# Optimization experiments

Hardware: AMD Instinct MI355X
Metric: run time of the kernel (lower is better)

Reference implementation:

```python
import jax, jax.numpy as jnp
import numpy as np


def setup_inputs() -> dict:
    key = jax.random.key(0)
    k1, k2 = jax.random.split(key)
    B, S, R, F = 256, 64, 128, 1536
    tri_feat_org = jax.random.normal(k1, (B, R, F), dtype=jnp.float32)
    alpha = jax.random.uniform(k2, (B, S, R), dtype=jnp.float32)
    mask = jnp.ones((B, S), dtype=jnp.float32)
    return {"tri_feat_org": tri_feat_org, "alpha": alpha, "mask": mask}


def reference(tri_feat_org, alpha, mask):
    # tri_feat_org: (B, R, 1536); alpha: (B, S, R); mask: (B, S)
    B, R, F = tri_feat_org.shape
    D = F // 6  # 256
    numtrue = jnp.sum(mask)
    # (alpha - 0.1) * mask, broadcast over rel dim (matches torch broadcasting;
    # the original's mask.expand_as(alpha) result is discarded)
    a = (alpha - 0.1) * mask[:, :, None]  # (B, S, R)

    # Slicing layout: h=[0:512], r=[512:1024], t=[1024:1536]; each split re/im 256
    h_re = tri_feat_org[..., 0 * D:1 * D]
    h_im = tri_feat_org[..., 1 * D:2 * D]
    r_re = tri_feat_org[..., 2 * D:3 * D]
    r_im = tri_feat_org[..., 3 * D:4 * D]
    t_re = tri_feat_org[..., 4 * D:5 * D]
    t_im = tri_feat_org[..., 5 * D:6 * D]

    # ComplEx score on the UNSCALED features; since alpha is constant across the
    # feature dim, (a*h)*(a*t)*(a*r) = a^3 * (h*t*r), so we never materialize
    # the (B,S,R,1536) expanded tensor the torch code builds.
    s0 = jnp.sum(h_re * t_re * r_re + h_im * t_im * r_re
                 + h_re * t_im * r_im - h_im * t_re * r_im, axis=-1)  # (B, R)
    score = -(a ** 3) * s0[:, None, :]  # (B, S, R)

    # regul: mean over (B,S,R,D) of (a * feat_slice)^2 for each of the 6 slices.
    # Factor as sum_{b,r} (sum_s a^2) * (sum_d feat^2) / (B*S*R*D).
    a2s = jnp.sum(a ** 2, axis=1)  # (B, R)
    S_len = a.shape[1]
    denom = jnp.asarray(B * S_len * R * D, dtype=tri_feat_org.dtype)

    def slice_mean_sq(f):
        return jnp.sum(a2s * jnp.sum(f ** 2, axis=-1)) / denom

    regul = (slice_mean_sq(h_re) + slice_mean_sq(h_im)
             + slice_mean_sq(t_re) + slice_mean_sq(t_im)
             + slice_mean_sq(r_re) + slice_mean_sq(r_im))

    output = jnp.sum(jax.nn.softplus(score)) / numtrue + 0.01 * regul
    return output
```

## Files before the change

### kernel.cpp

```cpp
#include <hip/hip_runtime.h>

constexpr int Bc = 256;
constexpr int Sc = 64;
constexpr int Rc = 128;
constexpr int Fc = 1536;
constexpr int Dc = 256;

__device__ __forceinline__ void accum_term(float h_re, float h_im,
                                           float r_re, float r_im,
                                           float t_re, float t_im,
                                           float& s0, float& q) {
  s0 += r_re * (h_re * t_re + h_im * t_im) + r_im * (h_re * t_im - h_im * t_re);
  q  += h_re * h_re + h_im * h_im + r_re * r_re + r_im * r_im + t_re * t_re + t_im * t_im;
}

__global__ __launch_bounds__(256) void rowstats_kernel(
    const float* __restrict__ tri, float* __restrict__ s0_out,
    float* __restrict__ q_out) {
  const int wid  = threadIdx.x >> 6;
  const int lane = threadIdx.x & 63;
  const int row  = blockIdx.x * 4 + wid;

  const float4* p4 = reinterpret_cast<const float4*>(tri + (size_t)row * Fc);
  const float4 hre = p4[lane +   0];
  const float4 him = p4[lane +  64];
  const float4 rre = p4[lane + 128];
  const float4 rim = p4[lane + 192];
  const float4 tre = p4[lane + 256];
  const float4 tim = p4[lane + 320];

  float s0 = 0.f, q = 0.f;
  accum_term(hre.x, him.x, rre.x, rim.x, tre.x, tim.x, s0, q);
  accum_term(hre.y, him.y, rre.y, rim.y, tre.y, tim.y, s0, q);
  accum_term(hre.z, him.z, rre.z, rim.z, tre.z, tim.z, s0, q);
  accum_term(hre.w, him.w, rre.w, rim.w, tre.w, tim.w, s0, q);

  #pragma unroll
  for (int off = 32; off > 0; off >>= 1) {
    s0 += __shfl_down(s0, off, 64);
    q  += __shfl_down(q, off, 64);
  }
  if (lane == 0) {
    s0_out[row] = s0;
    q_out[row]  = q;
  }
}

__global__ __launch_bounds__(256) void score_kernel(
    const float* __restrict__ alpha, const float* __restrict__ mask,
    const float* __restrict__ s0_arr, const float* __restrict__ q_arr,
    double* __restrict__ acc) {
  const int t   = blockIdx.x * 256 + threadIdx.x;
  const int idx = t * 4;
  const int r   = idx & (Rc - 1);
  const int bs  = idx >> 7;
  const int b   = bs >> 6;

  const float m = mask[bs];
  const float4 al  = *reinterpret_cast<const float4*>(alpha + idx);
  const float4 s0v = *reinterpret_cast<const float4*>(s0_arr + b * Rc + r);
  const float4 qv  = *reinterpret_cast<const float4*>(q_arr + b * Rc + r);

  float sp_sum = 0.f, aq_sum = 0.f;
  {
    float a = (al.x - 0.1f) * m;
    float sc = -(a * a * a) * s0v.x;
    sp_sum += fmaxf(sc, 0.f) + log1pf(__expf(-fabsf(sc)));
    aq_sum += a * a * qv.x;
  }
  {
    float a = (al.y - 0.1f) * m;
    float sc = -(a * a * a) * s0v.y;
    sp_sum += fmaxf(sc, 0.f) + log1pf(__expf(-fabsf(sc)));
    aq_sum += a * a * qv.y;
  }
  {
    float a = (al.z - 0.1f) * m;
    float sc = -(a * a * a) * s0v.z;
    sp_sum += fmaxf(sc, 0.f) + log1pf(__expf(-fabsf(sc)));
    aq_sum += a * a * qv.z;
  }
  {
    float a = (al.w - 0.1f) * m;
    float sc = -(a * a * a) * s0v.w;
    sp_sum += fmaxf(sc, 0.f) + log1pf(__expf(-fabsf(sc)));
    aq_sum += a * a * qv.w;
  }

  #pragma unroll
  for (int off = 32; off > 0; off >>= 1) {
    sp_sum += __shfl_down(sp_sum, off, 64);
    aq_sum += __shfl_down(aq_sum, off, 64);
  }
  __shared__ float lds[8];
  const int lane = threadIdx.x & 63, wid = threadIdx.x >> 6;
  if (lane == 0) {
    lds[wid]     = sp_sum;
    lds[wid + 4] = aq_sum;
  }
  __syncthreads();
  if (threadIdx.x == 0) {
    float spb = lds[0] + lds[1] + lds[2] + lds[3];
    float aqb = lds[4] + lds[5] + lds[6] + lds[7];
    atomicAdd(acc + 0, (double)spb);
    atomicAdd(acc + 1, (double)aqb);
  }
}

__global__ __launch_bounds__(256) void finalize_kernel(
    const float* __restrict__ mask, const double* __restrict__ acc,
    float* __restrict__ out) {
  float s = 0.f;
  for (int i = threadIdx.x; i < Bc * Sc; i += 256) s += mask[i];
  #pragma unroll
  for (int off = 32; off > 0; off >>= 1) s += __shfl_down(s, off, 64);
  __shared__ float lds[4];
  const int lane = threadIdx.x & 63, wid = threadIdx.x >> 6;
  if (lane == 0) lds[wid] = s;
  __syncthreads();
  if (threadIdx.x == 0) {
    double numtrue = (double)(lds[0] + lds[1] + lds[2] + lds[3]);
    double denom   = (double)Bc * (double)Sc * (double)Rc * (double)Dc;
    out[0] = (float)(acc[0] / numtrue + 0.01 * acc[1] / denom);
  }
}

extern "C" void kernel_launch(void* const* d_in, const int* in_sizes, int n_in,
                              void* d_out, int out_size, void* d_ws, size_t ws_size,
                              hipStream_t stream) {
  const float* tri   = (const float*)d_in[0];
  const float* alpha = (const float*)d_in[1];
  const float* mask  = (const float*)d_in[2];
  float* out = (float*)d_out;

  double* acc    = (double*)d_ws;
  float*  s0_arr = (float*)((char*)d_ws + 64);
  float*  q_arr  = s0_arr + Bc * Rc;

  hipMemsetAsync(d_ws, 0, 64, stream);

  rowstats_kernel<<<(Bc * Rc) / 4, 256, 0, stream>>>(tri, s0_arr, q_arr);
  score_kernel<<<(Bc * Sc * Rc) / (4 * 256), 256, 0, stream>>>(alpha, mask, s0_arr,
                                                               q_arr, acc);
  finalize_kernel<<<1, 256, 0, stream>>>(mask, acc, out);
}
```

Measured before the change: 342.5 us.

## Fuse rowstats, score and finalize into one kernel with last-block reduction

Merges the three kernels into a single launch. Each block computes row statistics for 16 relations of one batch into shared memory, then applies them to the matching alpha tile. The final mask sum and output are computed by the last block to finish, detected with an atomic counter. This removes the global intermediate arrays and two launch boundaries, at the cost of fewer blocks (2048), a serialized finalize tail, and per-block atomics.

```diff
diff --git a/kernel.cpp b/kernel.cpp
--- a/kernel.cpp
+++ b/kernel.cpp
@@ -5,6 +5,7 @@
 constexpr int Rc = 128;
 constexpr int Fc = 1536;
 constexpr int Dc = 256;
+
 
 __device__ __forceinline__ void accum_term(float h_re, float h_im,
                                            float r_re, float r_im,
@@ -14,77 +15,63 @@
   q  += h_re * h_re + h_im * h_im + r_re * r_re + r_im * r_im + t_re * t_re + t_im * t_im;
 }
 
-__global__ __launch_bounds__(256) void rowstats_kernel(
-    const float* __restrict__ tri, float* __restrict__ s0_out,
-    float* __restrict__ q_out) {
+__global__ __launch_bounds__(256) void fused_kernel(
+    const float* __restrict__ tri, const float* __restrict__ alpha,
+    const float* __restrict__ mask, double* __restrict__ acc,
+    unsigned int* __restrict__ counter, float* __restrict__ out) {
   const int wid  = threadIdx.x >> 6;
   const int lane = threadIdx.x & 63;
-  const int row  = blockIdx.x * 4 + wid;
+  const int b     = blockIdx.x >> 3;
+  const int r0    = (blockIdx.x & 7) * 16;
 
-  const float4* p4 = reinterpret_cast<const float4*>(tri + (size_t)row * Fc);
-  const float4 hre = p4[lane +   0];
-  const float4 him = p4[lane +  64];
-  const float4 rre = p4[lane + 128];
-  const float4 rim = p4[lane + 192];
-  const float4 tre = p4[lane + 256];
-  const float4 tim = p4[lane + 320];
-
-  float s0 = 0.f, q = 0.f;
-  accum_term(hre.x, him.x, rre.x, rim.x, tre.x, tim.x, s0, q);
-  accum_term(hre.y, him.y, rre.y, rim.y, tre.y, tim.y, s0, q);
-  accum_term(hre.z, him.z, rre.z, rim.z, tre.z, tim.z, s0, q);
-  accum_term(hre.w, him.w, rre.w, rim.w, tre.w, tim.w, s0, q);
+  __shared__ float s0_lds[16];
+  __shared__ float q_lds[16];
 
   #pragma unroll
-  for (int off = 32; off > 0; off >>= 1) {
-    s0 += __shfl_down(s0, off, 64);
-    q  += __shfl_down(q, off, 64);
+  for (int j = 0; j < 4; ++j) {
+    const int r = r0 + wid * 4 + j;
+    const float4* p4 =
+        reinterpret_cast<const float4*>(tri + ((size_t)b * Rc + r) * Fc);
+    const float4 hre = p4[lane +   0];
+    const float4 him = p4[lane +  64];
+    const float4 rre = p4[lane + 128];
+    const float4 rim = p4[lane + 192];
+    const float4 tre = p4[lane + 256];
+    const float4 tim = p4[lane + 320];
+
+    float s0 = 0.f, q = 0.f;
+    accum_term(hre.x, him.x, rre.x, rim.x, tre.x, tim.x, s0, q);
+    accum_term(hre.y, him.y, rre.y, rim.y, tre.y, tim.y, s0, q);
+    accum_term(hre.z, him.z, rre.z, rim.z, tre.z, tim.z, s0, q);
+    accum_term(hre.w, him.w, rre.w, rim.w, tre.w, tim.w, s0, q);
+
+    #pragma unroll
+    for (int off = 32; off > 0; off >>= 1) {
+      s0 += __shfl_down(s0, off, 64);
+      q  += __shfl_down(q, off, 64);
+    }
+    if (lane == 0) {
+      s0_lds[wid * 4 + j] = s0;
+      q_lds[wid * 4 + j]  = q;
+    }
   }
-  if (lane == 0) {
-    s0_out[row] = s0;
-    q_out[row]  = q;
-  }
-}
+  __syncthreads();
 
-__global__ __launch_bounds__(256) void score_kernel(
-    const float* __restrict__ alpha, const float* __restrict__ mask,
-    const float* __restrict__ s0_arr, const float* __restrict__ q_arr,
-    double* __restrict__ acc) {
-  const int t   = blockIdx.x * 256 + threadIdx.x;
-  const int idx = t * 4;
-  const int r   = idx & (Rc - 1);
-  const int bs  = idx >> 7;
-  const int b   = bs >> 6;
-
-  const float m = mask[bs];
-  const float4 al  = *reinterpret_cast<const float4*>(alpha + idx);
-  const float4 s0v = *reinterpret_cast<const float4*>(s0_arr + b * Rc + r);
-  const float4 qv  = *reinterpret_cast<const float4*>(q_arr + b * Rc + r);
+  const int s  = threadIdx.x >> 2;
+  const int rq = threadIdx.x & 3;
+  const float m = mask[b * Sc + s];
+  const float4 al = *reinterpret_cast<const float4*>(
+      alpha + ((size_t)b * Sc + s) * Rc + r0 + rq * 4);
 
   float sp_sum = 0.f, aq_sum = 0.f;
-  {
-    float a = (al.x - 0.1f) * m;
-    float sc = -(a * a * a) * s0v.x;
+  const float av[4] = {al.x, al.y, al.z, al.w};
+  #pragma unroll
+  for (int j = 0; j < 4; ++j) {
+    const int rl = rq * 4 + j;
+    const float a  = (av[j] - 0.1f) * m;
+    const float sc = -(a * a * a) * s0_lds[rl];
     sp_sum += fmaxf(sc, 0.f) + log1pf(__expf(-fabsf(sc)));
-    aq_sum += a * a * qv.x;
-  }
-  {
-    float a = (al.y - 0.1f) * m;
-    float sc = -(a * a * a) * s0v.y;
-    sp_sum += fmaxf(sc, 0.f) + log1pf(__expf(-fabsf(sc)));
-    aq_sum += a * a * qv.y;
-  }
-  {
-    float a = (al.z - 0.1f) * m;
-    float sc = -(a * a * a) * s0v.z;
-    sp_sum += fmaxf(sc, 0.f) + log1pf(__expf(-fabsf(sc)));
-    aq_sum += a * a * qv.z;
-  }
-  {
-    float a = (al.w - 0.1f) * m;
-    float sc = -(a * a * a) * s0v.w;
-    sp_sum += fmaxf(sc, 0.f) + log1pf(__expf(-fabsf(sc)));
-    aq_sum += a * a * qv.w;
+    aq_sum += a * a * q_lds[rl];
   }
 
   #pragma unroll
@@ -92,36 +79,39 @@
     sp_sum += __shfl_down(sp_sum, off, 64);
     aq_sum += __shfl_down(aq_sum, off, 64);
   }
-  __shared__ float lds[8];
-  const int lane = threadIdx.x & 63, wid = threadIdx.x >> 6;
+  __shared__ float red[8];
+  __shared__ bool last_block;
   if (lane == 0) {
-    lds[wid]     = sp_sum;
-    lds[wid + 4] = aq_sum;
+    red[wid]     = sp_sum;
+    red[wid + 4] = aq_sum;
   }
   __syncthreads();
   if (threadIdx.x == 0) {
-    float spb = lds[0] + lds[1] + lds[2] + lds[3];
-    float aqb = lds[4] + lds[5] + lds[6] + lds[7];
+    const float spb = red[0] + red[1] + red[2] + red[3];
+    const float aqb = red[4] + red[5] + red[6] + red[7];
     atomicAdd(acc + 0, (double)spb);
     atomicAdd(acc + 1, (double)aqb);
+    __threadfence();
+    const unsigned done = atomicAdd(counter, 1u);
+    last_block = (done == gridDim.x - 1);
   }
-}
+  __syncthreads();
 
-__global__ __launch_bounds__(256) void finalize_kernel(
-    const float* __restrict__ mask, const double* __restrict__ acc,
-    float* __restrict__ out) {
-  float s = 0.f;
-  for (int i = threadIdx.x; i < Bc * Sc; i += 256) s += mask[i];
-  #pragma unroll
-  for (int off = 32; off > 0; off >>= 1) s += __shfl_down(s, off, 64);
-  __shared__ float lds[4];
-  const int lane = threadIdx.x & 63, wid = threadIdx.x >> 6;
-  if (lane == 0) lds[wid] = s;
-  __syncthreads();
-  if (threadIdx.x == 0) {
-    double numtrue = (double)(lds[0] + lds[1] + lds[2] + lds[3]);
-    double denom   = (double)Bc * (double)Sc * (double)Rc * (double)Dc;
-    out[0] = (float)(acc[0] / numtrue + 0.01 * acc[1] / denom);
+  if (last_block) {
+    float msum = 0.f;
+    for (int i = threadIdx.x; i < Bc * Sc; i += 256) msum += mask[i];
+    #pragma unroll
+    for (int off = 32; off > 0; off >>= 1) msum += __shfl_down(msum, off, 64);
+    __shared__ float mred[4];
+    if (lane == 0) mred[wid] = msum;
+    __syncthreads();
+    if (threadIdx.x == 0) {
+      const double numtrue = (double)(mred[0] + mred[1] + mred[2] + mred[3]);
+      const double sp = atomicAdd(acc + 0, 0.0);
+      const double aq = atomicAdd(acc + 1, 0.0);
+      const double denom = (double)Bc * Sc * Rc * Dc;
+      out[0] = (float)(sp / numtrue + 0.01 * aq / denom);
+    }
   }
 }
 
@@ -133,14 +123,10 @@
   const float* mask  = (const float*)d_in[2];
   float* out = (float*)d_out;
 
-  double* acc    = (double*)d_ws;
-  float*  s0_arr = (float*)((char*)d_ws + 64);
-  float*  q_arr  = s0_arr + Bc * Rc;
+  double*       acc     = (double*)d_ws;
+  unsigned int* counter = (unsigned int*)((char*)d_ws + 16);
 
   hipMemsetAsync(d_ws, 0, 64, stream);
-
-  rowstats_kernel<<<(Bc * Rc) / 4, 256, 0, stream>>>(tri, s0_arr, q_arr);
-  score_kernel<<<(Bc * Sc * Rc) / (4 * 256), 256, 0, stream>>>(alpha, mask, s0_arr,
-                                                               q_arr, acc);
-  finalize_kernel<<<1, 256, 0, stream>>>(mask, acc, out);
+  fused_kernel<<<Bc * (Rc / 16), 256, 0, stream>>>(tri, alpha, mask, acc,
+                                                   counter, out);
 }
```

Result: slower. 388.3 us (+13.4%).
